# Optimization experiments

Hardware: AMD Instinct MI355X
Metric: run time of the kernel (lower is better)

The kernel has to match this reference:

```python
import jax, jax.numpy as jnp
import numpy as np

B, L, W, H = 4, 4096, 2048, 8
BW = W // H  # block width


def setup_inputs() -> dict:
    key = jax.random.key(0)
    k = jax.random.split(key, 5)
    std = 1.0 / np.sqrt(BW)  # w_init_variance_scale=1.0
    # a_param init: uniform ring in [0.9,0.999] then inverse-softplus
    u = jax.random.uniform(k[4], (W,), minval=0.9**2 + 1e-8, maxval=0.999**2 + 1e-8)
    a_param = jnp.log(jnp.exp(-0.5 * jnp.log(u)) - 1.0)
    return {
        "x": jax.random.normal(k[0], (B, L, W), dtype=jnp.float32),
        "segment_pos": jnp.arange(L, dtype=jnp.int32),
        "prev_h": jnp.zeros((B, W), dtype=jnp.float32),
        "ig_w": std * jax.random.normal(k[1], (H, BW, BW), dtype=jnp.float32),
        "ig_b": jnp.zeros((H, BW), dtype=jnp.float32),
        "ag_w": std * jax.random.normal(k[2], (H, BW, BW), dtype=jnp.float32),
        "ag_b": jnp.zeros((H, BW), dtype=jnp.float32),
        "a_param": a_param,
    }


@jax.custom_vjp
def sqrt_bound(x):
    return jnp.sqrt(x)

def _sb_fwd(x):
    return jnp.sqrt(x), x

def _sb_bwd(x, g):
    _MAX_SQRT_GRADIENT = 1000.0
    return (g / jnp.sqrt(jnp.clip(4.0 * x, 1.0 / _MAX_SQRT_GRADIENT**2)),)

sqrt_bound.defvjp(_sb_fwd, _sb_bwd)


def block_diag_linear(x, w, b):
    # x: [b,l,(h*i)] -> [b,l,h,i]; w: [h,i,j]; b: [h,j]
    bsz, l, _ = x.shape
    xr = x.reshape(bsz, l, H, BW)
    y = jnp.einsum("blhi,hij->blhj", xr, w) + b
    return y.reshape(bsz, l, W)


def reference(x, segment_pos, prev_h, ig_w, ig_b, ag_w, ag_b, a_param):
    reset = (segment_pos == 0)[None, :, None]  # [1,l,1] bool
    gate_x = jax.nn.sigmoid(block_diag_linear(x, ig_w, ig_b))
    gate_a = jax.nn.sigmoid(block_diag_linear(x, ag_w, ag_b))
    log_a = -8.0 * gate_a * jax.nn.softplus(a_param)  # [b,l,w]
    a = jnp.exp(log_a)
    a_square = jnp.exp(2.0 * log_a)
    gated_x = x * gate_x
    multiplier = sqrt_bound(1.0 - a_square)
    multiplier = jnp.where(reset, 1.0, multiplier)
    normalized_x = gated_x * multiplier.astype(x.dtype)
    a = a * (~reset)  # zero recurrence weight at document boundaries

    # linear scan h_t = a_t * h_{t-1} + x_t, accumulate in float32
    def step(h, inp):
        a_t, x_t = inp
        h = a_t.astype(jnp.float32) * h + x_t.astype(jnp.float32)
        return h, h.astype(x.dtype)

    a_t = jnp.swapaxes(jnp.broadcast_to(a, x.shape), 0, 1)  # [l,b,w]
    x_t = jnp.swapaxes(normalized_x, 0, 1)  # [l,b,w]
    last_h, y = jax.lax.scan(step, prev_h, (a_t, x_t))
    y = jnp.swapaxes(y, 0, 1)  # [b,l,w]
    return y, last_h
```

## Files before the change

### kernel.cpp

```cpp
#include <hip/hip_runtime.h>
#include <hip/hip_bf16.h>
#include <cmath>

#define Bq   4
#define Lq   4096
#define Wq   2048
#define Hq   8
#define Mq   (Bq*Lq)
#define RCH  128
#define NCH  (Lq/RCH)

typedef __bf16 bf16;
typedef __attribute__((ext_vector_type(8))) __bf16 bf16x8;
typedef __attribute__((ext_vector_type(4))) float  f32x4;

#define WS_WT    0
#define WS_C     (2*8*256*256*2)

__global__ __launch_bounds__(256) void prep2(const float* __restrict__ ig_w,
                                             const float* __restrict__ ag_w,
                                             const float* __restrict__ a_param,
                                             bf16* __restrict__ wt, float* __restrict__ c_arr) {
    __shared__ float t[64*65];
    int bid = blockIdx.x;
    int kt = bid & 3, nt = (bid >> 2) & 3, h = (bid >> 4) & 7, g = bid >> 7;
    const float* src = g ? ag_w : ig_w;
    int rr = threadIdx.x >> 6, cc = threadIdx.x & 63;
#pragma unroll
    for (int p = 0; p < 16; p++) {
        int kl = p*4 + rr;
        t[kl*65 + cc] = src[h*65536 + (kt*64 + kl)*256 + nt*64 + cc];
    }
    if (bid < 8) {
        float ap = a_param[bid*256 + threadIdx.x];
        c_arr[bid*256 + threadIdx.x] = 8.0f * log1pf(__expf(ap));
    }
    __syncthreads();
#pragma unroll
    for (int p = 0; p < 16; p++) {
        int nl = p*4 + rr;
        wt[((size_t)((g*8 + h)*256) + nt*64 + nl)*256 + kt*64 + cc] = (bf16)t[cc*65 + nl];
    }
}

__global__ __launch_bounds__(512, 1) void rglru_fused(
    const float* __restrict__ x, const int* __restrict__ segpos,
    const float* __restrict__ prev_h,
    const bf16* __restrict__ wt, const float* __restrict__ igb,
    const float* __restrict__ agb, const float* __restrict__ c_arr,
    float* __restrict__ out)
{
    __shared__ bf16x8 Wl[32*64];
    __shared__ float sgA[2][8][32], sgH[2][8][32];
    __shared__ float hc[2][32];

    const int tid = threadIdx.x;
    const int bid = blockIdx.x;
    const int h = bid & 7, b = (bid >> 3) & 3, s = bid >> 5;
    const int lane = tid & 63, wv = tid >> 6;
    const int l16 = lane & 15, quad = lane >> 4;
    const int wcol0 = h*256 + s*32;

    for (int t = tid; t < 2048; t += 512) {
        int ln = t & 63, ks = (t >> 6) & 7, ct = (t >> 9) & 1, g = t >> 10;
        int n  = s*32 + ct*16 + (ln & 15);
        int k  = ks*32 + (ln >> 4)*8;
        Wl[t] = *(const bf16x8*)&wt[((size_t)((g*8 + h)*256 + n))*256 + k];
    }
    float bxv[2], bav[2], ccv[2];
#pragma unroll
    for (int ct = 0; ct < 2; ct++) {
        int wf = wcol0 + ct*16 + l16;
        bxv[ct] = igb[wf]; bav[ct] = agb[wf]; ccv[ct] = c_arr[wf];
    }
    if (tid < 32) hc[0][tid] = prev_h[b*Wq + wcol0 + tid];

    const float* xfrag = x + ((size_t)b*Lq + wv*16 + l16)*Wq + h*256 + quad*8;
    const float* xgate = x + ((size_t)b*Lq + wv*16 + quad*4)*Wq + wcol0 + l16;
    const int*   spp   = segpos + wv*16 + quad*4;

    float4 xs[16]; float xg[8]; int sp[4];
#pragma unroll
    for (int ks = 0; ks < 8; ks++) {
        xs[2*ks]   = *(const float4*)(xfrag + ks*32);
        xs[2*ks+1] = *(const float4*)(xfrag + ks*32 + 4);
    }
#pragma unroll
    for (int r = 0; r < 4; r++) {
        sp[r] = spp[r];
#pragma unroll
        for (int ct = 0; ct < 2; ct++)
            xg[r*2+ct] = xgate[(size_t)r*Wq + ct*16];
    }
    __syncthreads();

    for (int c = 0; c < NCH; ++c) {
        const int cur = c & 1, nxt = cur ^ 1;
        const int cn  = (c < NCH-1) ? c+1 : c;

        f32x4 ax[2], aa[2];
#pragma unroll
        for (int j = 0; j < 2; j++) { ax[j] = (f32x4){0.f,0.f,0.f,0.f}; aa[j] = (f32x4){0.f,0.f,0.f,0.f}; }
#pragma unroll
        for (int ks = 0; ks < 8; ks++) {
            float4 u0 = xs[2*ks], u1 = xs[2*ks+1];
            bf16x8 af;
            af[0]=(bf16)u0.x; af[1]=(bf16)u0.y; af[2]=(bf16)u0.z; af[3]=(bf16)u0.w;
            af[4]=(bf16)u1.x; af[5]=(bf16)u1.y; af[6]=(bf16)u1.z; af[7]=(bf16)u1.w;
            bf16x8 w0 = Wl[(0*8+ks)*64 + lane];
            bf16x8 w1 = Wl[(1*8+ks)*64 + lane];
            bf16x8 w2 = Wl[(2*8+ks)*64 + lane];
            bf16x8 w3 = Wl[(3*8+ks)*64 + lane];
            ax[0] = __builtin_amdgcn_mfma_f32_16x16x32_bf16(af, w0, ax[0], 0,0,0);
            ax[1] = __builtin_amdgcn_mfma_f32_16x16x32_bf16(af, w1, ax[1], 0,0,0);
            aa[0] = __builtin_amdgcn_mfma_f32_16x16x32_bf16(af, w2, aa[0], 0,0,0);
            aa[1] = __builtin_amdgcn_mfma_f32_16x16x32_bf16(af, w3, aa[1], 0,0,0);
        }
        {
            const float* xp = xfrag + (size_t)cn*RCH*Wq;
#pragma unroll
            for (int ks = 0; ks < 8; ks++) {
                xs[2*ks]   = *(const float4*)(xp + ks*32);
                xs[2*ks+1] = *(const float4*)(xp + ks*32 + 4);
            }
        }

        float av[8], xn[8];
#pragma unroll
        for (int r = 0; r < 4; r++) {
            bool rst = (sp[r] == 0);
#pragma unroll
            for (int ct = 0; ct < 2; ct++) {
                float zx = ax[ct][r] + bxv[ct];
                float za = aa[ct][r] + bav[ct];
                float gx = __builtin_amdgcn_rcpf(1.f + __expf(-zx));
                float ga = __builtin_amdgcn_rcpf(1.f + __expf(-za));
                float a  = __expf(-ga * ccv[ct]);
                float mult = __builtin_amdgcn_sqrtf(fmaf(-a, a, 1.f));
                if (rst) { a = 0.f; mult = 1.f; }
                av[r*2+ct] = a;
                xn[r*2+ct] = gx * mult * xg[r*2+ct];
            }
        }
        {
            const float* xp = xgate + (size_t)cn*RCH*Wq;
#pragma unroll
            for (int r = 0; r < 4; r++) {
                sp[r] = spp[cn*RCH + r];
#pragma unroll
                for (int ct = 0; ct < 2; ct++)
                    xg[r*2+ct] = xp[(size_t)r*Wq + ct*16];
            }
        }

        float Pl[8], hl[8], Awv[2], Hwv[2];
#pragma unroll
        for (int ct = 0; ct < 2; ct++) {
            float A = 1.f, hv = 0.f;
#pragma unroll
            for (int r = 0; r < 4; r++) {
                hv = fmaf(av[r*2+ct], hv, xn[r*2+ct]);
                A *= av[r*2+ct];
                Pl[ct*4+r] = A; hl[ct*4+r] = hv;
            }
            float Asc = A, Hsc = hv;
            float Apv = __shfl(Asc, (lane-16) & 63), Hpv = __shfl(Hsc, (lane-16) & 63);
            if (quad >= 1) { Hsc = fmaf(Asc, Hpv, Hsc); Asc *= Apv; }
            Apv = __shfl(Asc, (lane-32) & 63); Hpv = __shfl(Hsc, (lane-32) & 63);
            if (quad >= 2) { Hsc = fmaf(Asc, Hpv, Hsc); Asc *= Apv; }
            float Aex = __shfl(Asc, (lane-16) & 63), Hex = __shfl(Hsc, (lane-16) & 63);
            if (quad == 0) { Aex = 1.f; Hex = 0.f; }
#pragma unroll
            for (int r = 0; r < 4; r++) {
                hl[ct*4+r] = fmaf(Pl[ct*4+r], Hex, hl[ct*4+r]);
                Pl[ct*4+r] *= Aex;
            }
            Awv[ct] = Asc; Hwv[ct] = Hsc;
            if (quad == 3) { sgA[cur][wv][ct*16+l16] = Asc; sgH[cur][wv][ct*16+l16] = Hsc; }
        }
        __syncthreads();

#pragma unroll
        for (int ct = 0; ct < 2; ct++) {
            int col = ct*16 + l16;
            float h0 = hc[cur][col];
#pragma unroll
            for (int w = 0; w < 7; w++)
                if (w < wv) h0 = fmaf(sgA[cur][w][col], h0, sgH[cur][w][col]);
            float* yp = out + ((size_t)b*Lq + (size_t)c*RCH + wv*16 + quad*4)*Wq + wcol0 + col;
#pragma unroll
            for (int r = 0; r < 4; r++)
                yp[(size_t)r*Wq] = fmaf(Pl[ct*4+r], h0, hl[ct*4+r]);
            if (wv == 7 && quad == 3)
                hc[nxt][col] = fmaf(Awv[ct], h0, Hwv[ct]);
        }
    }
    __syncthreads();
    if (tid < 32) out[(size_t)Mq*Wq + b*Wq + wcol0 + tid] = hc[NCH & 1][tid];
}

extern "C" void kernel_launch(void* const* d_in, const int* in_sizes, int n_in,
                              void* d_out, int out_size, void* d_ws, size_t ws_size,
                              hipStream_t stream) {
    const float* x       = (const float*)d_in[0];
    const int*   segpos  = (const int*)  d_in[1];
    const float* prev_h  = (const float*)d_in[2];
    const float* ig_w    = (const float*)d_in[3];
    const float* ig_b    = (const float*)d_in[4];
    const float* ag_w    = (const float*)d_in[5];
    const float* ag_b    = (const float*)d_in[6];
    const float* a_param = (const float*)d_in[7];
    float* out = (float*)d_out;

    char* ws = (char*)d_ws;
    bf16*   wt    = (bf16*)  (ws + WS_WT);
    float*  c_arr = (float*) (ws + WS_C);

    prep2<<<256, 256, 0, stream>>>(ig_w, ag_w, a_param, wt, c_arr);
    rglru_fused<<<256, 512, 0, stream>>>(x, segpos, prev_h, wt, ig_b, ag_b, c_arr, out);
}
```

Baseline: 366.5 us.

## Halve columns per block and double grid size for more parallelism

Each block of the fused RG-LRU kernel now owns 16 output columns instead of 32, and the grid grows from 256 to 512 blocks. Per-block MFMA, gate and scan work are halved, with launch bounds raised to allow up to 4 blocks per CU. The goal is to spread the serial chunk loop across more concurrent waves to hide latency. In exchange, each block re-reads the full 256-wide x fragment for the GEMM, doubling redundant x traffic. The tighter register budget implied by the new launch bounds may also force spills of the large prefetch buffer.

```diff
diff --git a/kernel.cpp b/kernel.cpp
--- a/kernel.cpp
+++ b/kernel.cpp
@@ -43,43 +43,39 @@
     }
 }
 
-__global__ __launch_bounds__(512, 1) void rglru_fused(
+__global__ __launch_bounds__(512, 4) void rglru_fused(
     const float* __restrict__ x, const int* __restrict__ segpos,
     const float* __restrict__ prev_h,
     const bf16* __restrict__ wt, const float* __restrict__ igb,
     const float* __restrict__ agb, const float* __restrict__ c_arr,
     float* __restrict__ out)
 {
-    __shared__ bf16x8 Wl[32*64];
-    __shared__ float sgA[2][8][32], sgH[2][8][32];
-    __shared__ float hc[2][32];
+    __shared__ bf16x8 Wl[16*64];
+    __shared__ float sgA[2][8][16], sgH[2][8][16];
+    __shared__ float hc[2][16];
 
     const int tid = threadIdx.x;
     const int bid = blockIdx.x;
     const int h = bid & 7, b = (bid >> 3) & 3, s = bid >> 5;
     const int lane = tid & 63, wv = tid >> 6;
     const int l16 = lane & 15, quad = lane >> 4;
-    const int wcol0 = h*256 + s*32;
+    const int wcol0 = h*256 + s*16;
 
-    for (int t = tid; t < 2048; t += 512) {
-        int ln = t & 63, ks = (t >> 6) & 7, ct = (t >> 9) & 1, g = t >> 10;
-        int n  = s*32 + ct*16 + (ln & 15);
+    for (int t = tid; t < 1024; t += 512) {
+        int ln = t & 63, ks = (t >> 6) & 7, g = t >> 9;
+        int n  = s*16 + (ln & 15);
         int k  = ks*32 + (ln >> 4)*8;
         Wl[t] = *(const bf16x8*)&wt[((size_t)((g*8 + h)*256 + n))*256 + k];
     }
-    float bxv[2], bav[2], ccv[2];
-#pragma unroll
-    for (int ct = 0; ct < 2; ct++) {
-        int wf = wcol0 + ct*16 + l16;
-        bxv[ct] = igb[wf]; bav[ct] = agb[wf]; ccv[ct] = c_arr[wf];
-    }
-    if (tid < 32) hc[0][tid] = prev_h[b*Wq + wcol0 + tid];
+    const int wf = wcol0 + l16;
+    const float bxv = igb[wf], bav = agb[wf], ccv = c_arr[wf];
+    if (tid < 16) hc[0][tid] = prev_h[b*Wq + wcol0 + tid];
 
     const float* xfrag = x + ((size_t)b*Lq + wv*16 + l16)*Wq + h*256 + quad*8;
     const float* xgate = x + ((size_t)b*Lq + wv*16 + quad*4)*Wq + wcol0 + l16;
     const int*   spp   = segpos + wv*16 + quad*4;
 
-    float4 xs[16]; float xg[8]; int sp[4];
+    float4 xs[16]; float xg[4]; int sp[4];
 #pragma unroll
     for (int ks = 0; ks < 8; ks++) {
         xs[2*ks]   = *(const float4*)(xfrag + ks*32);
@@ -88,9 +84,7 @@
 #pragma unroll
     for (int r = 0; r < 4; r++) {
         sp[r] = spp[r];
-#pragma unroll
-        for (int ct = 0; ct < 2; ct++)
-            xg[r*2+ct] = xgate[(size_t)r*Wq + ct*16];
+        xg[r] = xgate[(size_t)r*Wq];
     }
     __syncthreads();
 
@@ -98,9 +92,8 @@
         const int cur = c & 1, nxt = cur ^ 1;
         const int cn  = (c < NCH-1) ? c+1 : c;
 
-        f32x4 ax[2], aa[2];
-#pragma unroll
-        for (int j = 0; j < 2; j++) { ax[j] = (f32x4){0.f,0.f,0.f,0.f}; aa[j] = (f32x4){0.f,0.f,0.f,0.f}; }
+        f32x4 ax = (f32x4){0.f,0.f,0.f,0.f};
+        f32x4 aa = (f32x4){0.f,0.f,0.f,0.f};
 #pragma unroll
         for (int ks = 0; ks < 8; ks++) {
             float4 u0 = xs[2*ks], u1 = xs[2*ks+1];
@@ -109,12 +102,8 @@
             af[4]=(bf16)u1.x; af[5]=(bf16)u1.y; af[6]=(bf16)u1.z; af[7]=(bf16)u1.w;
             bf16x8 w0 = Wl[(0*8+ks)*64 + lane];
             bf16x8 w1 = Wl[(1*8+ks)*64 + lane];
-            bf16x8 w2 = Wl[(2*8+ks)*64 + lane];
-            bf16x8 w3 = Wl[(3*8+ks)*64 + lane];
-            ax[0] = __builtin_amdgcn_mfma_f32_16x16x32_bf16(af, w0, ax[0], 0,0,0);
-            ax[1] = __builtin_amdgcn_mfma_f32_16x16x32_bf16(af, w1, ax[1], 0,0,0);
-            aa[0] = __builtin_amdgcn_mfma_f32_16x16x32_bf16(af, w2, aa[0], 0,0,0);
-            aa[1] = __builtin_amdgcn_mfma_f32_16x16x32_bf16(af, w3, aa[1], 0,0,0);
+            ax = __builtin_amdgcn_mfma_f32_16x16x32_bf16(af, w0, ax, 0,0,0);
+            aa = __builtin_amdgcn_mfma_f32_16x16x32_bf16(af, w1, aa, 0,0,0);
         }
         {
             const float* xp = xfrag + (size_t)cn*RCH*Wq;
@@ -125,78 +114,66 @@
             }
         }
 
-        float av[8], xn[8];
+        float av[4], xn[4];
 #pragma unroll
         for (int r = 0; r < 4; r++) {
             bool rst = (sp[r] == 0);
-#pragma unroll
-            for (int ct = 0; ct < 2; ct++) {
-                float zx = ax[ct][r] + bxv[ct];
-                float za = aa[ct][r] + bav[ct];
-                float gx = __builtin_amdgcn_rcpf(1.f + __expf(-zx));
-                float ga = __builtin_amdgcn_rcpf(1.f + __expf(-za));
-                float a  = __expf(-ga * ccv[ct]);
-                float mult = __builtin_amdgcn_sqrtf(fmaf(-a, a, 1.f));
-                if (rst) { a = 0.f; mult = 1.f; }
-                av[r*2+ct] = a;
-                xn[r*2+ct] = gx * mult * xg[r*2+ct];
-            }
+            float zx = ax[r] + bxv;
+            float za = aa[r] + bav;
+            float gx = __builtin_amdgcn_rcpf(1.f + __expf(-zx));
+            float ga = __builtin_amdgcn_rcpf(1.f + __expf(-za));
+            float a  = __expf(-ga * ccv);
+            float mult = __builtin_amdgcn_sqrtf(fmaf(-a, a, 1.f));
+            if (rst) { a = 0.f; mult = 1.f; }
+            av[r] = a;
+            xn[r] = gx * mult * xg[r];
         }
         {
             const float* xp = xgate + (size_t)cn*RCH*Wq;
+            const int*   spn = spp + cn*RCH;
 #pragma unroll
             for (int r = 0; r < 4; r++) {
-                sp[r] = spp[cn*RCH + r];
-#pragma unroll
-                for (int ct = 0; ct < 2; ct++)
-                    xg[r*2+ct] = xp[(size_t)r*Wq + ct*16];
+                sp[r] = spn[r];
+                xg[r] = xp[(size_t)r*Wq];
             }
         }
 
-        float Pl[8], hl[8], Awv[2], Hwv[2];
+        float Pl[4], hl[4];
+        float A = 1.f, hv = 0.f;
 #pragma unroll
-        for (int ct = 0; ct < 2; ct++) {
-            float A = 1.f, hv = 0.f;
+        for (int r = 0; r < 4; r++) {
+            hv = fmaf(av[r], hv, xn[r]);
+            A *= av[r];
+            Pl[r] = A; hl[r] = hv;
+        }
+        float Asc = A, Hsc = hv;
+        float Apv = __shfl(Asc, (lane-16) & 63), Hpv = __shfl(Hsc, (lane-16) & 63);
+        if (quad >= 1) { Hsc = fmaf(Asc, Hpv, Hsc); Asc *= Apv; }
+        Apv = __shfl(Asc, (lane-32) & 63); Hpv = __shfl(Hsc, (lane-32) & 63);
+        if (quad >= 2) { Hsc = fmaf(Asc, Hpv, Hsc); Asc *= Apv; }
+        float Aex = __shfl(Asc, (lane-16) & 63), Hex = __shfl(Hsc, (lane-16) & 63);
+        if (quad == 0) { Aex = 1.f; Hex = 0.f; }
 #pragma unroll
-            for (int r = 0; r < 4; r++) {
-                hv = fmaf(av[r*2+ct], hv, xn[r*2+ct]);
-                A *= av[r*2+ct];
-                Pl[ct*4+r] = A; hl[ct*4+r] = hv;
-            }
-            float Asc = A, Hsc = hv;
-            float Apv = __shfl(Asc, (lane-16) & 63), Hpv = __shfl(Hsc, (lane-16) & 63);
-            if (quad >= 1) { Hsc = fmaf(Asc, Hpv, Hsc); Asc *= Apv; }
-            Apv = __shfl(Asc, (lane-32) & 63); Hpv = __shfl(Hsc, (lane-32) & 63);
-            if (quad >= 2) { Hsc = fmaf(Asc, Hpv, Hsc); Asc *= Apv; }
-            float Aex = __shfl(Asc, (lane-16) & 63), Hex = __shfl(Hsc, (lane-16) & 63);
-            if (quad == 0) { Aex = 1.f; Hex = 0.f; }
-#pragma unroll
-            for (int r = 0; r < 4; r++) {
-                hl[ct*4+r] = fmaf(Pl[ct*4+r], Hex, hl[ct*4+r]);
-                Pl[ct*4+r] *= Aex;
-            }
-            Awv[ct] = Asc; Hwv[ct] = Hsc;
-            if (quad == 3) { sgA[cur][wv][ct*16+l16] = Asc; sgH[cur][wv][ct*16+l16] = Hsc; }
+        for (int r = 0; r < 4; r++) {
+            hl[r] = fmaf(Pl[r], Hex, hl[r]);
+            Pl[r] *= Aex;
         }
+        if (quad == 3) { sgA[cur][wv][l16] = Asc; sgH[cur][wv][l16] = Hsc; }
         __syncthreads();
 
+        float h0 = hc[cur][l16];
 #pragma unroll
-        for (int ct = 0; ct < 2; ct++) {
-            int col = ct*16 + l16;
-            float h0 = hc[cur][col];
+        for (int w = 0; w < 7; w++)
+            if (w < wv) h0 = fmaf(sgA[cur][w][l16], h0, sgH[cur][w][l16]);
+        float* yp = out + ((size_t)b*Lq + (size_t)c*RCH + wv*16 + quad*4)*Wq + wcol0 + l16;
 #pragma unroll
-            for (int w = 0; w < 7; w++)
-                if (w < wv) h0 = fmaf(sgA[cur][w][col], h0, sgH[cur][w][col]);
-            float* yp = out + ((size_t)b*Lq + (size_t)c*RCH + wv*16 + quad*4)*Wq + wcol0 + col;
-#pragma unroll
-            for (int r = 0; r < 4; r++)
-                yp[(size_t)r*Wq] = fmaf(Pl[ct*4+r], h0, hl[ct*4+r]);
-            if (wv == 7 && quad == 3)
-                hc[nxt][col] = fmaf(Awv[ct], h0, Hwv[ct]);
-        }
+        for (int r = 0; r < 4; r++)
+            yp[(size_t)r*Wq] = fmaf(Pl[r], h0, hl[r]);
+        if (wv == 7 && quad == 3)
+            hc[nxt][l16] = fmaf(Asc, h0, Hsc);
     }
     __syncthreads();
-    if (tid < 32) out[(size_t)Mq*Wq + b*Wq + wcol0 + tid] = hc[NCH & 1][tid];
+    if (tid < 16) out[(size_t)Mq*Wq + b*Wq + wcol0 + tid] = hc[NCH & 1][tid];
 }
 
 extern "C" void kernel_launch(void* const* d_in, const int* in_sizes, int n_in,
@@ -217,5 +194,5 @@
     float*  c_arr = (float*) (ws + WS_C);
 
     prep2<<<256, 256, 0, stream>>>(ig_w, ag_w, a_param, wt, c_arr);
-    rglru_fused<<<256, 512, 0, stream>>>(x, segpos, prev_h, wt, ig_b, ag_b, c_arr, out);
+    rglru_fused<<<512, 512, 0, stream>>>(x, segpos, prev_h, wt, ig_b, ag_b, c_arr, out);
 }
```

Measured after the change: 500.5 us. 1.37x slower.

## Split fused kernel into parallel gate computation and packed-intermediate scan

Applied to the files above, without the earlier changes.

Splits the single fused kernel into two. A gate kernel with 512 blocks computes the block-diagonal matmul and gates over all rows in parallel. It writes each (normalized x, a) pair packed into 32 bits: x rounded to bf16 and a quantized to 16-bit fixed point. A separate scan kernel reads the packed values and does the chunked linear recurrence. This lets the matmul phase run independently of the sequential scan. The costs are an extra intermediate write and read through global memory and lower precision for both the decay a and the scanned input.

```diff
diff --git a/kernel.cpp b/kernel.cpp
--- a/kernel.cpp
+++ b/kernel.cpp
@@ -16,6 +16,7 @@
 
 #define WS_WT    0
 #define WS_C     (2*8*256*256*2)
+#define WS_PH    (4u<<20)
 
 __global__ __launch_bounds__(256) void prep2(const float* __restrict__ ig_w,
                                              const float* __restrict__ ag_w,
@@ -43,20 +44,17 @@
     }
 }
 
-__global__ __launch_bounds__(512, 1) void rglru_fused(
+__global__ __launch_bounds__(512, 4) void gates_pack(
     const float* __restrict__ x, const int* __restrict__ segpos,
-    const float* __restrict__ prev_h,
     const bf16* __restrict__ wt, const float* __restrict__ igb,
     const float* __restrict__ agb, const float* __restrict__ c_arr,
-    float* __restrict__ out)
+    unsigned* __restrict__ PH)
 {
     __shared__ bf16x8 Wl[32*64];
-    __shared__ float sgA[2][8][32], sgH[2][8][32];
-    __shared__ float hc[2][32];
 
     const int tid = threadIdx.x;
     const int bid = blockIdx.x;
-    const int h = bid & 7, b = (bid >> 3) & 3, s = bid >> 5;
+    const int h = bid >> 6, s = (bid >> 3) & 7, mq = bid & 7;
     const int lane = tid & 63, wv = tid >> 6;
     const int l16 = lane & 15, quad = lane >> 4;
     const int wcol0 = h*256 + s*32;
@@ -73,40 +71,27 @@
         int wf = wcol0 + ct*16 + l16;
         bxv[ct] = igb[wf]; bav[ct] = agb[wf]; ccv[ct] = c_arr[wf];
     }
-    if (tid < 32) hc[0][tid] = prev_h[b*Wq + wcol0 + tid];
-
-    const float* xfrag = x + ((size_t)b*Lq + wv*16 + l16)*Wq + h*256 + quad*8;
-    const float* xgate = x + ((size_t)b*Lq + wv*16 + quad*4)*Wq + wcol0 + l16;
-    const int*   spp   = segpos + wv*16 + quad*4;
-
-    float4 xs[16]; float xg[8]; int sp[4];
-#pragma unroll
-    for (int ks = 0; ks < 8; ks++) {
-        xs[2*ks]   = *(const float4*)(xfrag + ks*32);
-        xs[2*ks+1] = *(const float4*)(xfrag + ks*32 + 4);
-    }
-#pragma unroll
-    for (int r = 0; r < 4; r++) {
-        sp[r] = spp[r];
-#pragma unroll
-        for (int ct = 0; ct < 2; ct++)
-            xg[r*2+ct] = xgate[(size_t)r*Wq + ct*16];
-    }
-    __syncthreads();
-
-    for (int c = 0; c < NCH; ++c) {
-        const int cur = c & 1, nxt = cur ^ 1;
-        const int cn  = (c < NCH-1) ? c+1 : c;
-
+    __syncthreads();
+
+    const int mb0 = mq*2048;
+#pragma unroll 1
+    for (int it = 0; it < 16; ++it) {
+        const int mb = mb0 + it*128;
+        const float* xf = x + ((size_t)(mb + wv*16 + l16))*Wq + h*256 + quad*8;
+        float4 u0[8], u1[8];
+#pragma unroll
+        for (int ks = 0; ks < 8; ks++) {
+            u0[ks] = *(const float4*)(xf + ks*32);
+            u1[ks] = *(const float4*)(xf + ks*32 + 4);
+        }
         f32x4 ax[2], aa[2];
 #pragma unroll
         for (int j = 0; j < 2; j++) { ax[j] = (f32x4){0.f,0.f,0.f,0.f}; aa[j] = (f32x4){0.f,0.f,0.f,0.f}; }
 #pragma unroll
         for (int ks = 0; ks < 8; ks++) {
-            float4 u0 = xs[2*ks], u1 = xs[2*ks+1];
             bf16x8 af;
-            af[0]=(bf16)u0.x; af[1]=(bf16)u0.y; af[2]=(bf16)u0.z; af[3]=(bf16)u0.w;
-            af[4]=(bf16)u1.x; af[5]=(bf16)u1.y; af[6]=(bf16)u1.z; af[7]=(bf16)u1.w;
+            af[0]=(bf16)u0[ks].x; af[1]=(bf16)u0[ks].y; af[2]=(bf16)u0[ks].z; af[3]=(bf16)u0[ks].w;
+            af[4]=(bf16)u1[ks].x; af[5]=(bf16)u1[ks].y; af[6]=(bf16)u1[ks].z; af[7]=(bf16)u1[ks].w;
             bf16x8 w0 = Wl[(0*8+ks)*64 + lane];
             bf16x8 w1 = Wl[(1*8+ks)*64 + lane];
             bf16x8 w2 = Wl[(2*8+ks)*64 + lane];
@@ -116,19 +101,15 @@
             aa[0] = __builtin_amdgcn_mfma_f32_16x16x32_bf16(af, w2, aa[0], 0,0,0);
             aa[1] = __builtin_amdgcn_mfma_f32_16x16x32_bf16(af, w3, aa[1], 0,0,0);
         }
-        {
-            const float* xp = xfrag + (size_t)cn*RCH*Wq;
-#pragma unroll
-            for (int ks = 0; ks < 8; ks++) {
-                xs[2*ks]   = *(const float4*)(xp + ks*32);
-                xs[2*ks+1] = *(const float4*)(xp + ks*32 + 4);
-            }
-        }
-
-        float av[8], xn[8];
+
+        const int grow = mb + wv*16 + quad*4;
+        const float* xg = x + (size_t)grow*Wq + wcol0 + l16;
+        int4 sp = *(const int4*)(segpos + (grow & (Lq-1)));
+        int spv[4]; spv[0]=sp.x; spv[1]=sp.y; spv[2]=sp.z; spv[3]=sp.w;
+        unsigned* pp = PH + (size_t)grow*Wq + wcol0 + l16;
 #pragma unroll
         for (int r = 0; r < 4; r++) {
-            bool rst = (sp[r] == 0);
+            bool rst = (spv[r] == 0);
 #pragma unroll
             for (int ct = 0; ct < 2; ct++) {
                 float zx = ax[ct][r] + bxv[ct];
@@ -138,20 +119,47 @@
                 float a  = __expf(-ga * ccv[ct]);
                 float mult = __builtin_amdgcn_sqrtf(fmaf(-a, a, 1.f));
                 if (rst) { a = 0.f; mult = 1.f; }
-                av[r*2+ct] = a;
-                xn[r*2+ct] = gx * mult * xg[r*2+ct];
-            }
-        }
-        {
-            const float* xp = xgate + (size_t)cn*RCH*Wq;
-#pragma unroll
-            for (int r = 0; r < 4; r++) {
-                sp[r] = spp[cn*RCH + r];
-#pragma unroll
-                for (int ct = 0; ct < 2; ct++)
-                    xg[r*2+ct] = xp[(size_t)r*Wq + ct*16];
-            }
-        }
+                float xn = gx * mult * xg[(size_t)r*Wq + ct*16];
+                unsigned xb = __float_as_uint(xn);
+                xb = (xb + 0x7FFFu + ((xb >> 16) & 1u)) & 0xFFFF0000u;
+                unsigned au = (unsigned)fmaf(a, 65535.f, 0.5f);
+                pp[(size_t)r*Wq + ct*16] = xb | au;
+            }
+        }
+    }
+}
+
+__global__ __launch_bounds__(512, 4) void scan_apply(
+    const unsigned* __restrict__ PH, const float* __restrict__ prev_h,
+    float* __restrict__ out)
+{
+    __shared__ float sgA[2][8][32], sgH[2][8][32];
+    __shared__ float hc[2][32];
+
+    const int tid = threadIdx.x;
+    const int bid = blockIdx.x;
+    const int h = bid & 7, b = (bid >> 3) & 3, s = bid >> 5;
+    const int lane = tid & 63, wv = tid >> 6;
+    const int l16 = lane & 15, quad = lane >> 4;
+    const int wcol0 = h*256 + s*32;
+
+    if (tid < 32) hc[0][tid] = prev_h[b*Wq + wcol0 + tid];
+    __syncthreads();
+
+    for (int c = 0; c < NCH; ++c) {
+        const int cur = c & 1, nxt = cur ^ 1;
+        const int grow = b*Lq + c*RCH + wv*16 + quad*4;
+        const unsigned* pp = PH + (size_t)grow*Wq + wcol0 + l16;
+
+        float av[8], xn[8];
+#pragma unroll
+        for (int r = 0; r < 4; r++)
+#pragma unroll
+            for (int ct = 0; ct < 2; ct++) {
+                unsigned pk = pp[(size_t)r*Wq + ct*16];
+                xn[r*2+ct] = __uint_as_float(pk & 0xFFFF0000u);
+                av[r*2+ct] = (float)(pk & 0xFFFFu) * (1.0f/65535.0f);
+            }
 
         float Pl[8], hl[8], Awv[2], Hwv[2];
 #pragma unroll
@@ -187,7 +195,7 @@
 #pragma unroll
             for (int w = 0; w < 7; w++)
                 if (w < wv) h0 = fmaf(sgA[cur][w][col], h0, sgH[cur][w][col]);
-            float* yp = out + ((size_t)b*Lq + (size_t)c*RCH + wv*16 + quad*4)*Wq + wcol0 + col;
+            float* yp = out + (size_t)grow*Wq + wcol0 + col;
 #pragma unroll
             for (int r = 0; r < 4; r++)
                 yp[(size_t)r*Wq] = fmaf(Pl[ct*4+r], h0, hl[ct*4+r]);
@@ -213,9 +221,11 @@
     float* out = (float*)d_out;
 
     char* ws = (char*)d_ws;
-    bf16*   wt    = (bf16*)  (ws + WS_WT);
-    float*  c_arr = (float*) (ws + WS_C);
+    bf16*     wt    = (bf16*)    (ws + WS_WT);
+    float*    c_arr = (float*)   (ws + WS_C);
+    unsigned* PH    = (unsigned*)(ws + WS_PH);
 
     prep2<<<256, 256, 0, stream>>>(ig_w, ag_w, a_param, wt, c_arr);
-    rglru_fused<<<256, 512, 0, stream>>>(x, segpos, prev_h, wt, ig_b, ag_b, c_arr, out);
-}
+    gates_pack<<<512, 512, 0, stream>>>(x, segpos, wt, ig_b, ag_b, c_arr, PH);
+    scan_apply<<<256, 512, 0, stream>>>(PH, prev_h, out);
+}
```

New measurement: 547.5 us. 1.49x slower.
